# Kernel tuning notes

Measured on AMD Instinct MI355X. Metric: run time of the kernel, lower is better.

Reference implementation:

```python
import jax, jax.numpy as jnp
import numpy as np

B, S, HID = 2, 2048, 2048
N_HEADS = 16
HEAD_DIM = HID // N_HEADS  # 128
ROPE_THETA = 10000.0
MAX_SEQ = 4096


def _rope_cache(position_ids, head_dim, theta=ROPE_THETA, max_seq=MAX_SEQ):
    # standard RoPE cache: cos/sin of shape [B, S, head_dim//2]
    half = head_dim // 2
    inv_freq = 1.0 / theta ** (jnp.arange(half, dtype=jnp.float32) / half)
    t = jnp.arange(max_seq, dtype=jnp.float32)
    freqs = jnp.outer(t, inv_freq)                      # [max_seq, half]
    pos = jnp.clip(position_ids, 0, max_seq - 1)
    return jnp.cos(freqs)[pos], jnp.sin(freqs)[pos]     # [B, S, half]


def _apply_rope(q, k, cos, sin):
    # q,k: [B, H, S, D]; cos/sin: [B, S, D/2] -> [B, 1, S, D/2]
    cos = cos[:, None, :, :]
    sin = sin[:, None, :, :]
    q1, q2 = jnp.split(q, 2, axis=-1)
    k1, k2 = jnp.split(k, 2, axis=-1)
    q_rot = jnp.concatenate([q1 * cos - q2 * sin, q2 * cos + q1 * sin], axis=-1)
    k_rot = jnp.concatenate([k1 * cos - k2 * sin, k2 * cos + k1 * sin], axis=-1)
    return q_rot, k_rot


def setup_inputs() -> dict:
    key = jax.random.key(0)
    ks = jax.random.split(key, 6)
    hidden_states = jax.random.normal(ks[0], (B, S, HID), dtype=jnp.float32)
    # additive causal mask, broadcastable over batch and heads
    causal = jnp.tril(jnp.ones((S, S), dtype=bool))
    attention_mask = jnp.where(causal, 0.0, -1e9).astype(jnp.float32)[None, None]
    position_ids = jnp.broadcast_to(jnp.arange(S, dtype=jnp.int32)[None, :], (B, S))
    scale = 0.02
    Wq = jax.random.normal(ks[1], (HID, N_HEADS * HEAD_DIM), dtype=jnp.float32) * scale
    Wk = jax.random.normal(ks[2], (HID, N_HEADS * HEAD_DIM), dtype=jnp.float32) * scale
    Wv = jax.random.normal(ks[3], (HID, N_HEADS * HEAD_DIM), dtype=jnp.float32) * scale
    Wo = jax.random.normal(ks[4], (N_HEADS * HEAD_DIM, HID), dtype=jnp.float32) * scale
    zeros = jnp.zeros((HID,), dtype=jnp.float32)
    return {
        "hidden_states": hidden_states,
        "attention_mask": attention_mask,
        "position_ids": position_ids,
        "Wq": Wq, "bq": zeros,
        "Wk": Wk, "bk": zeros,
        "Wv": Wv, "bv": zeros,
        "Wo": Wo, "bo": zeros,
    }


def reference(hidden_states, attention_mask, position_ids,
              Wq, bq, Wk, bk, Wv, bv, Wo, bo):
    b, s, _ = hidden_states.shape
    q = (hidden_states @ Wq + bq).reshape(b, s, N_HEADS, HEAD_DIM).transpose(0, 2, 1, 3)
    k = (hidden_states @ Wk + bk).reshape(b, s, N_HEADS, HEAD_DIM).transpose(0, 2, 1, 3)
    v = (hidden_states @ Wv + bv).reshape(b, s, N_HEADS, HEAD_DIM).transpose(0, 2, 1, 3)

    cos, sin = _rope_cache(position_ids, HEAD_DIM)
    q, k = _apply_rope(q, k, cos, sin)

    scores = jnp.einsum("bhqd,bhkd->bhqk", q, k) / jnp.sqrt(jnp.float32(HEAD_DIM))
    scores = scores + attention_mask
    weights = jax.nn.softmax(scores, axis=-1)
    attn = jnp.einsum("bhqk,bhkd->bhqd", weights, v)  # [B,H,S,D]
    attn = attn.transpose(0, 2, 1, 3).reshape(b, s, N_HEADS * HEAD_DIM)
    return attn @ Wo + bo
```

## Files before the change

kernel.cpp:

```cpp
#include <hip/hip_runtime.h>
#include <hip/hip_bf16.h>

typedef __bf16 bf16;
typedef bf16 bf16x4 __attribute__((ext_vector_type(4)));
typedef bf16 bf16x8 __attribute__((ext_vector_type(8)));
typedef float f32x4 __attribute__((ext_vector_type(4)));

#define B_ 2
#define S_ 2048
#define HID_ 2048
#define NH_ 16
#define HD_ 128
#define M_TOT (B_ * S_)
#define RSCALE 0.08838834764831845f
#define LN10000_OVER_64 0.14391156f

#define OFF_XB   0ull
#define OFF_WQT  (OFF_XB  + (size_t)M_TOT*HID_*2)
#define OFF_WKT  (OFF_WQT + (size_t)HID_*HID_*2)
#define OFF_WVT  (OFF_WKT + (size_t)HID_*HID_*2)
#define OFF_WOT  (OFF_WVT + (size_t)HID_*HID_*2)
#define OFF_QB   (OFF_WOT + (size_t)HID_*HID_*2)
#define OFF_KB   (OFF_QB  + (size_t)M_TOT*HID_*2)
#define OFF_VTB  (OFF_KB  + (size_t)M_TOT*HID_*2)
#define OFF_AB   (OFF_VTB + (size_t)M_TOT*HID_*2)

__device__ __forceinline__ void gload16(const bf16* g, bf16* l) {
    typedef const __attribute__((address_space(1))) unsigned int gu32;
    typedef __attribute__((address_space(3))) unsigned int lu32;
    __builtin_amdgcn_global_load_lds((gu32*)g, (lu32*)l, 16, 0, 0);
}

__global__ __launch_bounds__(256) void cvt_x(const float* __restrict__ x,
                                             bf16* __restrict__ o) {
    size_t i = ((size_t)blockIdx.x * 256 + threadIdx.x) * 4;
    float4 v = *(const float4*)(x + i);
    bf16x4 r; r[0] = (bf16)v.x; r[1] = (bf16)v.y; r[2] = (bf16)v.z; r[3] = (bf16)v.w;
    *(bf16x4*)(o + i) = r;
}

__global__ __launch_bounds__(256) void trans_w(const float* w0, const float* w1,
                                               const float* w2, const float* w3,
                                               bf16* o0, bf16* o1, bf16* o2, bf16* o3) {
    const float* W; bf16* O;
    switch (blockIdx.z) {
        case 0: W = w0; O = o0; break;
        case 1: W = w1; O = o1; break;
        case 2: W = w2; O = o2; break;
        default: W = w3; O = o3; break;
    }
    __shared__ float t[64][65];
    int tid = threadIdx.x;
    int nt0 = blockIdx.x * 64, kt0 = blockIdx.y * 64;
    #pragma unroll
    for (int p = 0; p < 4; ++p) {
        int r = p * 16 + (tid >> 4);
        int c = (tid & 15) * 4;
        float4 v = *(const float4*)(W + (size_t)(kt0 + r) * HID_ + nt0 + c);
        t[r][c + 0] = v.x; t[r][c + 1] = v.y; t[r][c + 2] = v.z; t[r][c + 3] = v.w;
    }
    __syncthreads();
    #pragma unroll
    for (int p = 0; p < 4; ++p) {
        int rr = p * 16 + (tid >> 4);
        int cc = (tid & 15) * 4;
        bf16x4 v;
        v[0] = (bf16)t[cc + 0][rr]; v[1] = (bf16)t[cc + 1][rr];
        v[2] = (bf16)t[cc + 2][rr]; v[3] = (bf16)t[cc + 3][rr];
        *(bf16x4*)(O + (size_t)(nt0 + rr) * HID_ + kt0 + cc) = v;
    }
}

__global__ __launch_bounds__(256) void gemm_qkv(const bf16* __restrict__ A,
                                                const bf16* __restrict__ Wt3,
                                                const float* __restrict__ bq,
                                                const float* __restrict__ bk,
                                                const float* __restrict__ bv,
                                                const int* __restrict__ pos_ids,
                                                bf16* __restrict__ out3) {
    __shared__ bf16 Al[128][64];
    __shared__ bf16 Bl[128][64];
    const int tid = threadIdx.x;
    const int l = tid & 63, w = tid >> 6;
    const int ln = l & 15, lg = l >> 4;
    const int bm = blockIdx.y;
    const int sel = blockIdx.x >> 4, bnn = blockIdx.x & 15;
    const bf16* Bt = Wt3 + (size_t)sel * HID_ * HID_ + (size_t)bnn * 128 * HID_;
    const float* bias = sel == 0 ? bq : (sel == 1 ? bk : bv);
    const int swz = (ln & 7) * 8;

    f32x4 acc[2][8] = {};

    for (int k0 = 0; k0 < HID_; k0 += 64) {
        __syncthreads();
        #pragma unroll
        for (int j = 0; j < 4; ++j) {
            int r0 = w * 32 + j * 8;
            int r = r0 + (l >> 3);
            int c = (((l & 7) ^ ((l >> 3) & 7))) * 8;
            gload16(A  + (size_t)(bm * 128 + r) * HID_ + k0 + c, &Al[r0][0]);
            gload16(Bt + (size_t)r * HID_ + k0 + c, &Bl[r0][0]);
        }
        __syncthreads();
        #pragma unroll
        for (int kk = 0; kk < 2; ++kk) {
            bf16x8 af[2], bfv[8];
            #pragma unroll
            for (int fm = 0; fm < 2; ++fm)
                af[fm] = *(const bf16x8*)&Al[w * 32 + fm * 16 + ln][(kk * 32 + lg * 8) ^ swz];
            #pragma unroll
            for (int fn = 0; fn < 8; ++fn)
                bfv[fn] = *(const bf16x8*)&Bl[fn * 16 + ln][(kk * 32 + lg * 8) ^ swz];
            #pragma unroll
            for (int fm = 0; fm < 2; ++fm)
                #pragma unroll
                for (int fn = 0; fn < 8; ++fn)
                    acc[fm][fn] = __builtin_amdgcn_mfma_f32_16x16x32_bf16(
                        af[fm], bfv[fn], acc[fm][fn], 0, 0, 0);
        }
    }

    #pragma unroll
    for (int fm = 0; fm < 2; ++fm) {
        #pragma unroll
        for (int i = 0; i < 4; ++i) {
            int m_g = bm * 128 + w * 32 + fm * 16 + lg * 4 + i;
            int b = m_g >> 11, s = m_g & (S_ - 1);
            if (sel == 2) {
                bf16* O = out3 + 2 * (size_t)M_TOT * HID_;
                #pragma unroll
                for (int fn = 0; fn < 8; ++fn) {
                    int d = fn * 16 + ln;
                    float v = acc[fm][fn][i] + bias[bnn * 128 + d];
                    O[((size_t)(b * NH_ + bnn) * HD_ + d) * S_ + s] = (bf16)v;
                }
            } else {
                int pos = pos_ids[m_g];
                pos = pos < 0 ? 0 : (pos > 4095 ? 4095 : pos);
                size_t base = ((size_t)(b * NH_ + bnn) * S_ + s) * HD_;
                bf16* O = out3 + (size_t)sel * M_TOT * HID_;
                #pragma unroll
                for (int fn = 0; fn < 4; ++fn) {
                    int j = fn * 16 + ln;
                    float x1 = acc[fm][fn][i]     + bias[bnn * 128 + j];
                    float x2 = acc[fm][fn + 4][i] + bias[bnn * 128 + j + 64];
                    float invf = __expf(-(float)j * LN10000_OVER_64);
                    float ang = (float)pos * invf;
                    float sn, cs;
                    __sincosf(ang, &sn, &cs);
                    float y1 = x1 * cs - x2 * sn;
                    float y2 = x2 * cs + x1 * sn;
                    if (sel == 0) { y1 *= RSCALE; y2 *= RSCALE; }
                    O[base + j]      = (bf16)y1;
                    O[base + j + 64] = (bf16)y2;
                }
            }
        }
    }
}

__global__ __launch_bounds__(256) void gemm_o(const bf16* __restrict__ A,
                                              const bf16* __restrict__ Bt,
                                              const float* __restrict__ bias,
                                              float* __restrict__ out) {
    __shared__ bf16 Al[128][64];
    __shared__ bf16 Bl[128][64];
    const int tid = threadIdx.x;
    const int l = tid & 63, w = tid >> 6;
    const int ln = l & 15, lg = l >> 4;
    const int bm = blockIdx.y, bn = blockIdx.x;
    const int swz = (ln & 7) * 8;

    f32x4 acc[2][8] = {};

    for (int k0 = 0; k0 < HID_; k0 += 64) {
        __syncthreads();
        #pragma unroll
        for (int j = 0; j < 4; ++j) {
            int r0 = w * 32 + j * 8;
            int r = r0 + (l >> 3);
            int c = (((l & 7) ^ ((l >> 3) & 7))) * 8;
            gload16(A  + (size_t)(bm * 128 + r) * HID_ + k0 + c, &Al[r0][0]);
            gload16(Bt + (size_t)(bn * 128 + r) * HID_ + k0 + c, &Bl[r0][0]);
        }
        __syncthreads();
        #pragma unroll
        for (int kk = 0; kk < 2; ++kk) {
            bf16x8 af[2], bfv[8];
            #pragma unroll
            for (int fm = 0; fm < 2; ++fm)
                af[fm] = *(const bf16x8*)&Al[w * 32 + fm * 16 + ln][(kk * 32 + lg * 8) ^ swz];
            #pragma unroll
            for (int fn = 0; fn < 8; ++fn)
                bfv[fn] = *(const bf16x8*)&Bl[fn * 16 + ln][(kk * 32 + lg * 8) ^ swz];
            #pragma unroll
            for (int fm = 0; fm < 2; ++fm)
                #pragma unroll
                for (int fn = 0; fn < 8; ++fn)
                    acc[fm][fn] = __builtin_amdgcn_mfma_f32_16x16x32_bf16(
                        af[fm], bfv[fn], acc[fm][fn], 0, 0, 0);
        }
    }

    #pragma unroll
    for (int fm = 0; fm < 2; ++fm)
        #pragma unroll
        for (int i = 0; i < 4; ++i) {
            int m_g = bm * 128 + w * 32 + fm * 16 + lg * 4 + i;
            #pragma unroll
            for (int fn = 0; fn < 8; ++fn) {
                int n_g = bn * 128 + fn * 16 + ln;
                out[(size_t)m_g * HID_ + n_g] = acc[fm][fn][i] + bias[n_g];
            }
        }
}

__global__ __launch_bounds__(512) void attn_k(const bf16* __restrict__ Q,
                                              const bf16* __restrict__ K,
                                              const bf16* __restrict__ Vt,
                                              bf16* __restrict__ O) {
    __shared__ bf16 Kl[2][64][128];
    __shared__ bf16 Vl[2][128][64];
    __shared__ bf16 Pl[8][16][64];
    const int tid = threadIdx.x;
    const int l = tid & 63, w = tid >> 6;
    const int ln = l & 15, lg = l >> 4;
    const int bid = blockIdx.x;
    const int j  = 15 - (bid >> 5);
    const int bh = bid & 31;
    const int nkt = 2 * j + 2;

    const bf16* Qb = Q  + (size_t)bh * S_ * HD_;
    const bf16* Kb = K  + (size_t)bh * S_ * HD_;
    const bf16* Vb = Vt + (size_t)bh * S_ * HD_;
    const int b = bh >> 4, h = bh & (NH_ - 1);

    const int qrow = j * 128 + w * 16 + ln;
    const int qg0  = j * 128 + w * 16 + lg * 4;
    const int fK = tid, rK = fK >> 4, cK = fK & 15;
    const int swzP = (ln & 7) * 8;

    bf16x8 qf[4];
    #pragma unroll
    for (int kk = 0; kk < 4; ++kk)
        qf[kk] = *(const bf16x8*)(Qb + (size_t)qrow * HD_ + kk * 32 + lg * 8);

    float m_run[4], l_run[4];
    #pragma unroll
    for (int i = 0; i < 4; ++i) { m_run[i] = -1e30f; l_run[i] = 0.f; }
    f32x4 oacc[8] = {};

    uint4 kr[2], vr[2];
    #pragma unroll
    for (int m = 0; m < 2; ++m) {
        int f = m * 512 + tid;
        kr[m] = *(const uint4*)(Kb + (size_t)(f >> 4) * HD_ + (f & 15) * 8);
        vr[m] = *(const uint4*)(Vb + (size_t)(f >> 3) * S_ + (f & 7) * 8);
    }
    #pragma unroll
    for (int m = 0; m < 2; ++m) {
        int f = m * 512 + tid;
        int r = f >> 4,  c = f & 15;
        int rv = f >> 3, cv = f & 7;
        *(uint4*)&Kl[0][r][(c ^ (r & 7)) * 8] = kr[m];
        *(uint4*)&Vl[0][rv][(cv ^ (rv & 7)) * 8] = vr[m];
    }
    if (nkt > 1) {
        #pragma unroll
        for (int m = 0; m < 2; ++m) {
            int f = m * 512 + tid;
            kr[m] = *(const uint4*)(Kb + (size_t)(64 + (f >> 4)) * HD_ + (f & 15) * 8);
            vr[m] = *(const uint4*)(Vb + (size_t)(f >> 3) * S_ + 64 + (f & 7) * 8);
        }
    }
    __syncthreads();

    for (int kt = 0; kt < nkt; ++kt) {
        const int cur = kt & 1;
        if (kt + 1 < nkt) {
            #pragma unroll
            for (int m = 0; m < 2; ++m) {
                int f = m * 512 + tid;
                int r = f >> 4,  c = f & 15;
                int rv = f >> 3, cv = f & 7;
                *(uint4*)&Kl[cur ^ 1][r][(c ^ (r & 7)) * 8] = kr[m];
                *(uint4*)&Vl[cur ^ 1][rv][(cv ^ (rv & 7)) * 8] = vr[m];
            }
        }
        if (kt + 2 < nkt) {
            #pragma unroll
            for (int m = 0; m < 2; ++m) {
                int f = m * 512 + tid;
                kr[m] = *(const uint4*)(Kb + (size_t)((kt + 2) * 64 + (f >> 4)) * HD_ + (f & 15) * 8);
                vr[m] = *(const uint4*)(Vb + (size_t)(f >> 3) * S_ + (kt + 2) * 64 + (f & 7) * 8);
            }
        }

        f32x4 sacc[4] = {};
        __builtin_amdgcn_s_setprio(1);
        #pragma unroll
        for (int kk = 0; kk < 4; ++kk) {
            bf16x8 kf[4];
            #pragma unroll
            for (int n = 0; n < 4; ++n)
                kf[n] = *(const bf16x8*)&Kl[cur][n * 16 + ln][(kk * 32 + lg * 8) ^ swzP];
            #pragma unroll
            for (int n = 0; n < 4; ++n)
                sacc[n] = __builtin_amdgcn_mfma_f32_16x16x32_bf16(qf[kk], kf[n], sacc[n], 0, 0, 0);
        }
        __builtin_amdgcn_s_setprio(0);

        if (kt >= 2 * j) {
            #pragma unroll
            for (int n = 0; n < 4; ++n)
                #pragma unroll
                for (int i = 0; i < 4; ++i) {
                    int kg = kt * 64 + n * 16 + ln;
                    if (kg > qg0 + i) sacc[n][i] = -1e30f;
                }
        }

        float mt[4];
        #pragma unroll
        for (int i = 0; i < 4; ++i) {
            mt[i] = fmaxf(fmaxf(sacc[0][i], sacc[1][i]), fmaxf(sacc[2][i], sacc[3][i]));
            #pragma unroll
            for (int d = 1; d < 16; d <<= 1)
                mt[i] = fmaxf(mt[i], __shfl_xor(mt[i], d));
        }
        float scale[4], rs[4];
        #pragma unroll
        for (int i = 0; i < 4; ++i) {
            float mnew = fmaxf(m_run[i], mt[i]);
            scale[i] = __expf(m_run[i] - mnew);
            m_run[i] = mnew;
            rs[i] = 0.f;
        }
        #pragma unroll
        for (int n = 0; n < 4; ++n)
            #pragma unroll
            for (int i = 0; i < 4; ++i) {
                float p = __expf(sacc[n][i] - m_run[i]);
                sacc[n][i] = p;
                rs[i] += p;
            }
        #pragma unroll
        for (int n = 0; n < 4; ++n)
            #pragma unroll
            for (int i = 0; i < 4; ++i)
                Pl[w][lg * 4 + i][(n * 16 + ln) ^ (((lg * 4 + i) & 7) * 8)] = (bf16)sacc[n][i];

        #pragma unroll
        for (int i = 0; i < 4; ++i) {
            #pragma unroll
            for (int d = 1; d < 16; d <<= 1)
                rs[i] += __shfl_xor(rs[i], d);
            l_run[i] = l_run[i] * scale[i] + rs[i];
        }
        #pragma unroll
        for (int dn = 0; dn < 8; ++dn)
            #pragma unroll
            for (int i = 0; i < 4; ++i)
                oacc[dn][i] *= scale[i];

        __builtin_amdgcn_s_setprio(1);
        #pragma unroll
        for (int kk = 0; kk < 2; ++kk) {
            bf16x8 pf = *(const bf16x8*)&Pl[w][ln][(kk * 32 + lg * 8) ^ swzP];
            #pragma unroll
            for (int dn = 0; dn < 8; ++dn) {
                bf16x8 vf = *(const bf16x8*)&Vl[cur][dn * 16 + ln][(kk * 32 + lg * 8) ^ swzP];
                oacc[dn] = __builtin_amdgcn_mfma_f32_16x16x32_bf16(pf, vf, oacc[dn], 0, 0, 0);
            }
        }
        __builtin_amdgcn_s_setprio(0);

        __syncthreads();
    }

    #pragma unroll
    for (int i = 0; i < 4; ++i) {
        float inv = 1.0f / l_run[i];
        int s = j * 128 + w * 16 + lg * 4 + i;
        #pragma unroll
        for (int dn = 0; dn < 8; ++dn) {
            int d = dn * 16 + ln;
            O[((size_t)(b * S_ + s)) * HID_ + h * HD_ + d] = (bf16)(oacc[dn][i] * inv);
        }
    }
}

extern "C" void kernel_launch(void* const* d_in, const int* in_sizes, int n_in,
                              void* d_out, int out_size, void* d_ws, size_t ws_size,
                              hipStream_t stream) {
    const float* X    = (const float*)d_in[0];
    const int*   pos  = (const int*)d_in[2];
    const float* Wq   = (const float*)d_in[3];
    const float* bq   = (const float*)d_in[4];
    const float* Wk   = (const float*)d_in[5];
    const float* bk   = (const float*)d_in[6];
    const float* Wv   = (const float*)d_in[7];
    const float* bv   = (const float*)d_in[8];
    const float* Wo   = (const float*)d_in[9];
    const float* bo   = (const float*)d_in[10];
    float* Out = (float*)d_out;

    char* ws = (char*)d_ws;
    bf16* Xb  = (bf16*)(ws + OFF_XB);
    bf16* Wqt = (bf16*)(ws + OFF_WQT);
    bf16* Wkt = (bf16*)(ws + OFF_WKT);
    bf16* Wvt = (bf16*)(ws + OFF_WVT);
    bf16* Wot = (bf16*)(ws + OFF_WOT);
    bf16* Qb  = (bf16*)(ws + OFF_QB);
    bf16* Kb  = (bf16*)(ws + OFF_KB);
    bf16* Vtb = (bf16*)(ws + OFF_VTB);
    bf16* Ab  = (bf16*)(ws + OFF_AB);

    cvt_x<<<(M_TOT * HID_) / (256 * 4), 256, 0, stream>>>(X, Xb);
    trans_w<<<dim3(32, 32, 4), 256, 0, stream>>>(Wq, Wk, Wv, Wo, Wqt, Wkt, Wvt, Wot);

    gemm_qkv<<<dim3(48, M_TOT / 128), 256, 0, stream>>>(Xb, Wqt, bq, bk, bv, pos, Qb);

    attn_k<<<dim3(512), 512, 0, stream>>>(Qb, Kb, Vtb, Ab);

    gemm_o<<<dim3(HID_ / 128, M_TOT / 128), 256, 0, stream>>>(Ab, Wot, bo, Out);
}
```

Measured before the change: 344.0 us.

## Remap GEMM blocks per XCD for L2 reuse and skip softmax rescales lazily

The QKV and output projection GEMMs now launch on a 1D grid and remap block ids so that each of the 8 XCDs owns a fixed subset of weight column tiles. This is meant to keep each weight tile resident in one XCD's L2 instead of being fetched by all of them. The attention kernel also gains a lazy online-softmax rescale: the running max, and with it the O and l accumulators, is only updated when some row's tile max exceeds the running max by more than 8. That removes per-tile exp and multiply work at the cost of a wave-wide vote and exponentials that may reach e^8 before normalization.

```diff
diff --git a/kernel.cpp b/kernel.cpp
--- a/kernel.cpp
+++ b/kernel.cpp
@@ -83,8 +83,11 @@
     const int tid = threadIdx.x;
     const int l = tid & 63, w = tid >> 6;
     const int ln = l & 15, lg = l >> 4;
-    const int bm = blockIdx.y;
-    const int sel = blockIdx.x >> 4, bnn = blockIdx.x & 15;
+    const int id = blockIdx.x;
+    const int xcd = id & 7, k = id >> 3;
+    const int pn = xcd * 6 + (k % 6);
+    const int bm = k / 6;
+    const int sel = pn >> 4, bnn = pn & 15;
     const bf16* Bt = Wt3 + (size_t)sel * HID_ * HID_ + (size_t)bnn * 128 * HID_;
     const float* bias = sel == 0 ? bq : (sel == 1 ? bk : bv);
     const int swz = (ln & 7) * 8;
@@ -160,7 +163,7 @@
 }
 
 __global__ __launch_bounds__(256) void gemm_o(const bf16* __restrict__ A,
-                                              const bf16* __restrict__ Bt,
+                                              const bf16* __restrict__ Bt0,
                                               const float* __restrict__ bias,
                                               float* __restrict__ out) {
     __shared__ bf16 Al[128][64];
@@ -168,7 +171,11 @@
     const int tid = threadIdx.x;
     const int l = tid & 63, w = tid >> 6;
     const int ln = l & 15, lg = l >> 4;
-    const int bm = blockIdx.y, bn = blockIdx.x;
+    const int id = blockIdx.x;
+    const int xcd = id & 7, k = id >> 3;
+    const int bn = xcd * 2 + (k & 1);
+    const int bm = k >> 1;
+    const bf16* Bt = Bt0 + (size_t)bn * 128 * HID_;
     const int swz = (ln & 7) * 8;
 
     f32x4 acc[2][8] = {};
@@ -181,7 +188,7 @@
             int r = r0 + (l >> 3);
             int c = (((l & 7) ^ ((l >> 3) & 7))) * 8;
             gload16(A  + (size_t)(bm * 128 + r) * HID_ + k0 + c, &Al[r0][0]);
-            gload16(Bt + (size_t)(bn * 128 + r) * HID_ + k0 + c, &Bl[r0][0]);
+            gload16(Bt + (size_t)r * HID_ + k0 + c, &Bl[r0][0]);
         }
         __syncthreads();
         #pragma unroll
@@ -237,7 +244,6 @@
 
     const int qrow = j * 128 + w * 16 + ln;
     const int qg0  = j * 128 + w * 16 + lg * 4;
-    const int fK = tid, rK = fK >> 4, cK = fK & 15;
     const int swzP = (ln & 7) * 8;
 
     bf16x8 qf[4];
@@ -328,14 +334,22 @@
             for (int d = 1; d < 16; d <<= 1)
                 mt[i] = fmaxf(mt[i], __shfl_xor(mt[i], d));
         }
-        float scale[4], rs[4];
-        #pragma unroll
-        for (int i = 0; i < 4; ++i) {
-            float mnew = fmaxf(m_run[i], mt[i]);
-            scale[i] = __expf(m_run[i] - mnew);
-            m_run[i] = mnew;
-            rs[i] = 0.f;
-        }
+        bool ok = true;
+        #pragma unroll
+        for (int i = 0; i < 4; ++i) ok = ok && (mt[i] <= m_run[i] + 8.f);
+        if (!__all(ok)) {
+            #pragma unroll
+            for (int i = 0; i < 4; ++i) {
+                float mnew = fmaxf(m_run[i], mt[i]);
+                float scale = __expf(m_run[i] - mnew);
+                m_run[i] = mnew;
+                l_run[i] *= scale;
+                #pragma unroll
+                for (int dn = 0; dn < 8; ++dn)
+                    oacc[dn][i] *= scale;
+            }
+        }
+        float rs[4] = {0.f, 0.f, 0.f, 0.f};
         #pragma unroll
         for (int n = 0; n < 4; ++n)
             #pragma unroll
@@ -355,13 +369,8 @@
             #pragma unroll
             for (int d = 1; d < 16; d <<= 1)
                 rs[i] += __shfl_xor(rs[i], d);
-            l_run[i] = l_run[i] * scale[i] + rs[i];
-        }
-        #pragma unroll
-        for (int dn = 0; dn < 8; ++dn)
-            #pragma unroll
-            for (int i = 0; i < 4; ++i)
-                oacc[dn][i] *= scale[i];
+            l_run[i] += rs[i];
+        }
 
         __builtin_amdgcn_s_setprio(1);
         #pragma unroll
@@ -419,9 +428,9 @@
     cvt_x<<<(M_TOT * HID_) / (256 * 4), 256, 0, stream>>>(X, Xb);
     trans_w<<<dim3(32, 32, 4), 256, 0, stream>>>(Wq, Wk, Wv, Wo, Wqt, Wkt, Wvt, Wot);
 
-    gemm_qkv<<<dim3(48, M_TOT / 128), 256, 0, stream>>>(Xb, Wqt, bq, bk, bv, pos, Qb);
+    gemm_qkv<<<dim3(1536), 256, 0, stream>>>(Xb, Wqt, bq, bk, bv, pos, Qb);
 
     attn_k<<<dim3(512), 512, 0, stream>>>(Qb, Kb, Vtb, Ab);
 
-    gemm_o<<<dim3(HID_ / 128, M_TOT / 128), 256, 0, stream>>>(Ab, Wot, bo, Out);
-}
+    gemm_o<<<dim3(512), 256, 0, stream>>>(Ab, Wot, bo, Out);
+}
```

After: 350.0 us. No clear change (+1.7%).
